# Performance work log

Hardware: AMD Instinct MI355X
Metric: run time of the kernel (lower is better)

## Reference

```python
import jax, jax.numpy as jnp
import numpy as np

LEAKY_SLOPE = 0.01  # torch nn.LeakyReLU default

def leaky_relu(x):
    return jnp.where(x >= 0, x, LEAKY_SLOPE * x)

def setup_inputs() -> dict:
    key = jax.random.key(0)
    ks = jax.random.split(key, 11)
    B, F, C_IN, H, K, D = 2048, 512, 3, 64, 8, 128  # batch, features, expand, layer_conf[0], bucket_num, bucket_dim
    ASR, MM, OUT = 128, 768, 256
    proj_in = ASR + MM + F * D
    inp = {
        "stat_features": jax.random.uniform(ks[0], (B, F), dtype=jnp.float32),
        "asr_embeddings": jax.random.normal(ks[1], (B, ASR), dtype=jnp.float32),
        "mm_embeddings": jax.random.normal(ks[2], (B, MM), dtype=jnp.float32),
        "linear1_w": jax.random.normal(ks[3], (F, C_IN, H), dtype=jnp.float32) * (1.0 / np.sqrt(C_IN)),
        "linear1_b": jax.random.normal(ks[4], (F, 1, H), dtype=jnp.float32),
        "linear2_w": jax.random.normal(ks[5], (F, H, K), dtype=jnp.float32) * (1.0 / np.sqrt(H)),
        "linear2_b": jax.random.normal(ks[6], (F, 1, K), dtype=jnp.float32),
        "tau": jnp.ones((F, 1, K), dtype=jnp.float32),
        "emb": jax.random.normal(ks[7], (F, K, D), dtype=jnp.float32),
        "proj_w": jax.random.normal(ks[8], (OUT, proj_in), dtype=jnp.float32) * (1.0 / np.sqrt(proj_in)),
        "proj_b": jax.random.normal(ks[9], (OUT,), dtype=jnp.float32) * 0.01,
    }
    return inp

def reference(stat_features, asr_embeddings, mm_embeddings,
              linear1_w, linear1_b, linear2_w, linear2_b, tau, emb,
              proj_w, proj_b):
    # sanitize: NaN -> 0, negatives -> 0
    x = stat_features
    x = jnp.where(jnp.isnan(x) | (x < 0.0), 0.0, x)  # [B, F]

    # auto_dis: per-feature tiny MLP. x is expanded to 3 identical copies -> [B,F,1,3]
    # matmul with [F,3,H] == einsum over the 3 copies.
    B, F = x.shape
    x3 = jnp.broadcast_to(x[:, :, None], (B, F, 3))           # [B,F,3]
    h = jnp.einsum('bfc,fch->bfh', x3, linear1_w) + linear1_b[:, 0, :]  # [B,F,H]
    h = jnp.where(h >= 0, h, LEAKY_SLOPE * h)
    s = jnp.einsum('bfh,fhk->bfk', h, linear2_w) + linear2_b[:, 0, :]   # [B,F,K]
    s = jnp.where(s >= 0, s, LEAKY_SLOPE * s)
    s = s * tau[:, 0, :]
    p = jax.nn.softmax(s, axis=-1)                            # [B,F,K]
    y = jnp.einsum('bfk,fkd->bfd', p, emb)                    # [B,F,D]
    y = y.reshape(B, -1)                                      # [B, F*D] (fc = Identity)

    z = jnp.concatenate([asr_embeddings, mm_embeddings, y], axis=1)
    out = jax.nn.relu(z @ proj_w.T + proj_b)                  # [B, 256]
    return out
```

## Files before the change

kernel.cpp:

```cpp
#include <hip/hip_runtime.h>
#include <hip/hip_bf16.h>
#include <math.h>

#define LEAKY 0.01f
#define B_    2048
#define F_    512
#define H_    64
#define K_    8
#define D_    128
#define ASR_  128
#define MM_   768
#define OUT_  256
#define PROJ_IN 66432
#define ZK    4992
#define NSPLIT 8


typedef unsigned short u16;
typedef u16   u16x8 __attribute__((ext_vector_type(8)));
typedef short s16x8 __attribute__((ext_vector_type(8)));
typedef float f32x4 __attribute__((ext_vector_type(4)));

__device__ __forceinline__ u16 f2bf(float x) {
  unsigned int u = __float_as_uint(x);
  u += 0x7fffu + ((u >> 16) & 1u);
  return (u16)(u >> 16);
}

#define PRODUCER_BLOCKS (512 + 1024 + 896 + 224)
#define PWS 132

__global__ __launch_bounds__(256) void producer_kernel(
    const float* __restrict__ stat, const float* __restrict__ w1,
    const float* __restrict__ b1v, const float* __restrict__ w2,
    const float* __restrict__ b2v, const float* __restrict__ tauv,
    const float* __restrict__ pw, const float* __restrict__ emb,
    const float* __restrict__ asr, const float* __restrict__ mm,
    u16* __restrict__ A0, u16* __restrict__ Pf, u16* __restrict__ Wn) {
  __shared__ __align__(16) char smem[15616];
  const int bid = blockIdx.x;
  const int t = threadIdx.x;

  if (bid < 512) {
    const int f0 = (bid >> 3) * 8;
    const int o0 = (bid & 7) * 32;
    float* s_pw = (float*)smem;
    const int fl = t >> 5, k = (t >> 2) & 7, dq = t & 3;
    float4 e[8];
    {
      const float* ep = emb + ((size_t)(f0 + fl) * 8 + k) * 128 + dq * 32;
      #pragma unroll
      for (int j = 0; j < 8; ++j) e[j] = *(const float4*)(ep + j * 4);
    }
    const int cf = t >> 5, cd = (t & 31) * 4;
    const float* pwbase = pw + 896 + (size_t)f0 * 128 + (size_t)(o0)*PROJ_IN + t * 4;
    float4 nxt = *(const float4*)(pwbase);
    for (int r = 0; r < 32; ++r) {
      float* buf = s_pw + (r & 1) * (8 * PWS);
      *(float4*)(buf + cf * PWS + cd) = nxt;
      __syncthreads();
      if (r + 1 < 32) nxt = *(const float4*)(pwbase + (size_t)(r + 1) * PROJ_IN);
      const float* pp = buf + fl * PWS + dq * 32;
      float g = 0.f;
      #pragma unroll
      for (int j = 0; j < 8; ++j) {
        float4 p4 = *(const float4*)(pp + j * 4);
        g = fmaf(e[j].x, p4.x, g);
        g = fmaf(e[j].y, p4.y, g);
        g = fmaf(e[j].z, p4.z, g);
        g = fmaf(e[j].w, p4.w, g);
      }
      g += __shfl_xor(g, 1);
      g += __shfl_xor(g, 2);
      if (dq == 0)
        Wn[(size_t)(o0 + r) * ZK + 896 + (f0 + fl) * 8 + k] = f2bf(g);
    }
  } else if (bid < 1536) {
    const int pb = bid - 512;
    const int f0 = (pb & 127) * 4;
    const int b0 = (pb >> 7) * 256;
    float* s_w1s = (float*)(smem);
    float* s_b1  = (float*)(smem + 1024);
    float* s_w2  = (float*)(smem + 2048);
    float* s_b2  = (float*)(smem + 10240);
    float* s_tau = (float*)(smem + 10368);
    float* s_x   = (float*)(smem + 10496);
    {
      int fl = t >> 6, h = t & 63;
      const float* wf = w1 + (size_t)(f0 + fl) * 192;
      s_w1s[fl * 64 + h] = wf[h] + wf[64 + h] + wf[128 + h];
      s_b1[fl * 64 + h] = b1v[(size_t)(f0 + fl) * 64 + h];
    }
    for (int i = t; i < 4 * 512; i += 256) {
      int fl = i >> 9, idx = i & 511;
      s_w2[fl * 512 + idx] = w2[(size_t)(f0 + fl) * 512 + idx];
    }
    if (t < 32) {
      s_b2[t]  = b2v[f0 * 8 + t];
      s_tau[t] = tauv[f0 * 8 + t];
    }
    for (int p = 0; p < 4; ++p) {
      int i = p * 256 + t;
      int r = i >> 2, fl = i & 3;
      float v = stat[(size_t)(b0 + r) * F_ + f0 + fl];
      s_x[r * 5 + fl] = (v >= 0.f) ? v : 0.f;
    }
    __syncthreads();

    const int w = t >> 6;
    const int lane = t & 63;
    const float* w1p = s_w1s + w * 64;
    const float* b1p = s_b1 + w * 64;
    const float* w2p = s_w2 + w * 512;
    float x[4];
    #pragma unroll
    for (int p = 0; p < 4; ++p) x[p] = s_x[(lane + 64 * p) * 5 + w];
    float acc[4][8] = {{0.f}};
    #pragma unroll 4
    for (int i = 0; i < 64; ++i) {
      float wv = w1p[i], bv = b1p[i];
      float4 wa = *(const float4*)(w2p + i * 8);
      float4 wb = *(const float4*)(w2p + i * 8 + 4);
      #pragma unroll
      for (int p = 0; p < 4; ++p) {
        float h0 = fmaf(x[p], wv, bv);
        float h = fmaf(LEAKY, fminf(h0, 0.f), fmaxf(h0, 0.f));
        acc[p][0] = fmaf(h, wa.x, acc[p][0]);
        acc[p][1] = fmaf(h, wa.y, acc[p][1]);
        acc[p][2] = fmaf(h, wa.z, acc[p][2]);
        acc[p][3] = fmaf(h, wa.w, acc[p][3]);
        acc[p][4] = fmaf(h, wb.x, acc[p][4]);
        acc[p][5] = fmaf(h, wb.y, acc[p][5]);
        acc[p][6] = fmaf(h, wb.z, acc[p][6]);
        acc[p][7] = fmaf(h, wb.w, acc[p][7]);
      }
    }
    #pragma unroll
    for (int p = 0; p < 4; ++p) {
      float s[K_];
      float m = -1e30f;
      #pragma unroll
      for (int kk = 0; kk < K_; ++kk) {
        float v = acc[p][kk] + s_b2[w * 8 + kk];
        v = (v >= 0.f) ? v : LEAKY * v;
        v *= s_tau[w * 8 + kk];
        s[kk] = v;
        m = fmaxf(m, v);
      }
      float sum = 0.f;
      #pragma unroll
      for (int kk = 0; kk < K_; ++kk) { s[kk] = __expf(s[kk] - m); sum += s[kk]; }
      float inv = 1.f / sum;
      u16x8 hv;
      #pragma unroll
      for (int kk = 0; kk < K_; ++kk) hv[kk] = f2bf(s[kk] * inv);
      *(u16x8*)(Pf + ((size_t)(f0 + w) * B_ + b0 + lane + 64 * p) * 8) = hv;
    }
  } else if (bid < 2432) {
    const int item = bid - 1536;
    const int cidx = item * 256 + t;
    const int r = cidx / 112, c = cidx % 112;
    float4 v0, v1;
    if (c < 16) {
      const float* s = asr + (size_t)r * ASR_ + c * 8;
      v0 = *(const float4*)(s); v1 = *(const float4*)(s + 4);
    } else {
      const float* s = mm + (size_t)r * MM_ + (c - 16) * 8;
      v0 = *(const float4*)(s); v1 = *(const float4*)(s + 4);
    }
    u16x8 hv = {f2bf(v0.x), f2bf(v0.y), f2bf(v0.z), f2bf(v0.w),
                f2bf(v1.x), f2bf(v1.y), f2bf(v1.z), f2bf(v1.w)};
    *(u16x8*)(A0 + (size_t)r * 896 + c * 8) = hv;
  } else {
    const int item = bid - 2432;
    #pragma unroll
    for (int rr = 0; rr < 4; ++rr) {
      int idx = item * 1024 + rr * 256 + t;
      int o = idx / 896, j = idx % 896;
      Wn[(size_t)o * ZK + j] = f2bf(pw[(size_t)o * PROJ_IN + j]);
    }
  }
}

#define SAS 72
__global__ __launch_bounds__(256) void gemm_kernel(
    const u16* __restrict__ A0, const u16* __restrict__ Pf,
    const u16* __restrict__ Wn, float* __restrict__ part) {
  const int bm0 = blockIdx.x * 64;
  const int bn0 = blockIdx.y * 64;
  const int kz  = blockIdx.z;
  const int it0 = kz * 10;
  const int itn = (kz == 7) ? 8 : 10;
  __shared__ u16 sA[64 * SAS];
  __shared__ u16 sB[64 * SAS];
  const int t = threadIdx.x;
  const int w = t >> 6, L = t & 63;
  const int l16 = L & 15, q8 = (L >> 4) * 8;
  const int wm = (w >> 1) * 32, wn = (w & 1) * 32;
  const int row = t >> 2, lk = t & 3;
  const int pp = t >> 5, pg = t & 31;
  f32x4 acc[2][2] = {{{0.f,0.f,0.f,0.f},{0.f,0.f,0.f,0.f}},
                     {{0.f,0.f,0.f,0.f},{0.f,0.f,0.f,0.f}}};
  u16x8 ra[2], rb[2];

#define LOAD_TILES(IT)                                                        \
  {                                                                           \
    const int k0_ = (IT) * 64;                                                \
    if (k0_ < 896) {                                                          \
      const u16* s_ = A0 + (size_t)(bm0 + row) * 896 + k0_ + lk * 8;          \
      ra[0] = *(const u16x8*)(s_);                                            \
      ra[1] = *(const u16x8*)(s_ + 32);                                       \
    } else {                                                                  \
      const int fb_ = (k0_ - 896) >> 3;                                       \
      const u16* s_ = Pf + ((size_t)(fb_ + pp) * B_ + bm0 + pg) * 8;          \
      ra[0] = *(const u16x8*)(s_);                                            \
      ra[1] = *(const u16x8*)(s_ + 256);                        \
    }                                                                         \
    const u16* sb_ = Wn + (size_t)(bn0 + row) * ZK + k0_ + lk * 8;            \
    rb[0] = *(const u16x8*)(sb_);                                             \
    rb[1] = *(const u16x8*)(sb_ + 32);                                        \
  }

#define STORE_TILES(IT)                                                       \
  {                                                                           \
    if ((IT) * 64 < 896) {                                                    \
      *(u16x8*)&sA[row * SAS + lk * 8]      = ra[0];                          \
      *(u16x8*)&sA[row * SAS + lk * 8 + 32] = ra[1];                          \
    } else {                                                                  \
      *(u16x8*)&sA[pg * SAS + pp * 8]        = ra[0];                         \
      *(u16x8*)&sA[(pg + 32) * SAS + pp * 8] = ra[1];                         \
    }                                                                         \
    *(u16x8*)&sB[row * SAS + lk * 8]      = rb[0];                            \
    *(u16x8*)&sB[row * SAS + lk * 8 + 32] = rb[1];                            \
  }

  LOAD_TILES(it0);
  for (int it = it0; it < it0 + itn; ++it) {
    __syncthreads();
    STORE_TILES(it);
    __syncthreads();
    if (it + 1 < it0 + itn) LOAD_TILES(it + 1);
    #pragma unroll
    for (int ks = 0; ks < 2; ++ks) {
      s16x8 a0 = *(const s16x8*)&sA[(wm + l16) * SAS + ks * 32 + q8];
      s16x8 a1 = *(const s16x8*)&sA[(wm + 16 + l16) * SAS + ks * 32 + q8];
      s16x8 b0 = *(const s16x8*)&sB[(wn + l16) * SAS + ks * 32 + q8];
      s16x8 b1 = *(const s16x8*)&sB[(wn + 16 + l16) * SAS + ks * 32 + q8];
      acc[0][0] = __builtin_amdgcn_mfma_f32_16x16x32_bf16(a0, b0, acc[0][0], 0, 0, 0);
      acc[0][1] = __builtin_amdgcn_mfma_f32_16x16x32_bf16(a0, b1, acc[0][1], 0, 0, 0);
      acc[1][0] = __builtin_amdgcn_mfma_f32_16x16x32_bf16(a1, b0, acc[1][0], 0, 0, 0);
      acc[1][1] = __builtin_amdgcn_mfma_f32_16x16x32_bf16(a1, b1, acc[1][1], 0, 0, 0);
    }
  }
#undef LOAD_TILES
#undef STORE_TILES

  float* dst = part + (size_t)kz * B_ * OUT_;
  #pragma unroll
  for (int mf = 0; mf < 2; ++mf) {
    const int r0 = bm0 + wm + mf * 16 + (L >> 4) * 4;
    #pragma unroll
    for (int nf = 0; nf < 2; ++nf) {
      const int col = bn0 + wn + nf * 16 + l16;
      #pragma unroll
      for (int i = 0; i < 4; ++i)
        dst[(size_t)(r0 + i) * OUT_ + col] = acc[mf][nf][i];
    }
  }
}

__global__ __launch_bounds__(256) void combine_kernel(
    const float* __restrict__ part, const float* __restrict__ pb,
    float* __restrict__ out) {
  const int idx4 = (blockIdx.x * 256 + threadIdx.x) * 4;
  const int o = idx4 & (OUT_ - 1);
  float4 bv = *(const float4*)(pb + o);
  float4 r = bv;
  #pragma unroll
  for (int kz = 0; kz < NSPLIT; ++kz) {
    float4 a = *(const float4*)(part + (size_t)kz * B_ * OUT_ + idx4);
    r.x += a.x; r.y += a.y; r.z += a.z; r.w += a.w;
  }
  r.x = r.x > 0.f ? r.x : 0.f;
  r.y = r.y > 0.f ? r.y : 0.f;
  r.z = r.z > 0.f ? r.z : 0.f;
  r.w = r.w > 0.f ? r.w : 0.f;
  *(float4*)(out + idx4) = r;
}

extern "C" void kernel_launch(void* const* d_in, const int* in_sizes, int n_in,
                              void* d_out, int out_size, void* d_ws, size_t ws_size,
                              hipStream_t stream) {
  (void)in_sizes; (void)n_in; (void)out_size; (void)ws_size;
  const float* stat = (const float*)d_in[0];
  const float* asr  = (const float*)d_in[1];
  const float* mm   = (const float*)d_in[2];
  const float* w1   = (const float*)d_in[3];
  const float* b1   = (const float*)d_in[4];
  const float* w2   = (const float*)d_in[5];
  const float* b2   = (const float*)d_in[6];
  const float* tau  = (const float*)d_in[7];
  const float* emb  = (const float*)d_in[8];
  const float* pw   = (const float*)d_in[9];
  const float* pb   = (const float*)d_in[10];
  float* out = (float*)d_out;
  char* ws = (char*)d_ws;
  u16*   A0   = (u16*)(ws);
  u16*   Pf   = (u16*)(ws + 3670016);
  u16*   Wn   = (u16*)(ws + 20447232);
  float* part = (float*)(ws + 23003136);

  producer_kernel<<<PRODUCER_BLOCKS, 256, 0, stream>>>(
      stat, w1, b1, w2, b2, tau, pw, emb, asr, mm, A0, Pf, Wn);
  gemm_kernel<<<dim3(B_ / 64, OUT_ / 64, NSPLIT), 256, 0, stream>>>(
      A0, Pf, Wn, part);
  combine_kernel<<<B_ * OUT_ / 1024, 256, 0, stream>>>(part, pb, out);
}
```

Before: 161.7 us.

## Fuse split-K combine into GEMM via atomic counters and split weight-fold blocks

Removes the separate combine kernel. Each GEMM tile increments a per-tile atomic counter, and the last split-K block for that tile sums the partials, adds bias, applies ReLU and writes the output. The weight-folding producer blocks are split into twice as many blocks with 16 outputs each. The shared-memory layout is padded per dq segment to reduce bank conflicts, and a trailing barrier is added. Counters are zeroed inside the producer kernel. This trades one launch and a full pass over the partials for atomics and fences.

Result: slower. 319.3 us (+97.5%).

```diff
diff --git a/kernel.cpp b/kernel.cpp
--- a/kernel.cpp
+++ b/kernel.cpp
@@ -27,8 +27,9 @@
   return (u16)(u >> 16);
 }
 
-#define PRODUCER_BLOCKS (512 + 1024 + 896 + 224)
-#define PWS 132
+#define PRODUCER_BLOCKS (1024 + 1024 + 896 + 224)
+#define DQS 36
+#define FLS 176
 
 __global__ __launch_bounds__(256) void producer_kernel(
     const float* __restrict__ stat, const float* __restrict__ w1,
@@ -36,14 +37,15 @@
     const float* __restrict__ b2v, const float* __restrict__ tauv,
     const float* __restrict__ pw, const float* __restrict__ emb,
     const float* __restrict__ asr, const float* __restrict__ mm,
-    u16* __restrict__ A0, u16* __restrict__ Pf, u16* __restrict__ Wn) {
+    u16* __restrict__ A0, u16* __restrict__ Pf, u16* __restrict__ Wn,
+    int* __restrict__ cnt) {
   __shared__ __align__(16) char smem[15616];
   const int bid = blockIdx.x;
   const int t = threadIdx.x;
 
-  if (bid < 512) {
-    const int f0 = (bid >> 3) * 8;
-    const int o0 = (bid & 7) * 32;
+  if (bid < 1024) {
+    const int f0 = (bid >> 4) * 8;
+    const int o0 = (bid & 15) * 16;
     float* s_pw = (float*)smem;
     const int fl = t >> 5, k = (t >> 2) & 7, dq = t & 3;
     float4 e[8];
@@ -52,15 +54,15 @@
       #pragma unroll
       for (int j = 0; j < 8; ++j) e[j] = *(const float4*)(ep + j * 4);
     }
-    const int cf = t >> 5, cd = (t & 31) * 4;
-    const float* pwbase = pw + 896 + (size_t)f0 * 128 + (size_t)(o0)*PROJ_IN + t * 4;
+    const int cf = t >> 5, dqs = (t & 31) >> 3, js = t & 7;
+    const float* pwbase = pw + 896 + (size_t)f0 * 128 + (size_t)o0 * PROJ_IN + t * 4;
     float4 nxt = *(const float4*)(pwbase);
-    for (int r = 0; r < 32; ++r) {
-      float* buf = s_pw + (r & 1) * (8 * PWS);
-      *(float4*)(buf + cf * PWS + cd) = nxt;
+    for (int r = 0; r < 16; ++r) {
+      float* buf = s_pw + (r & 1) * (8 * FLS);
+      *(float4*)(buf + cf * FLS + dqs * DQS + js * 4) = nxt;
       __syncthreads();
-      if (r + 1 < 32) nxt = *(const float4*)(pwbase + (size_t)(r + 1) * PROJ_IN);
-      const float* pp = buf + fl * PWS + dq * 32;
+      if (r + 1 < 16) nxt = *(const float4*)(pwbase + (size_t)(r + 1) * PROJ_IN);
+      const float* pp = buf + fl * FLS + dq * DQS;
       float g = 0.f;
       #pragma unroll
       for (int j = 0; j < 8; ++j) {
@@ -74,9 +76,10 @@
       g += __shfl_xor(g, 2);
       if (dq == 0)
         Wn[(size_t)(o0 + r) * ZK + 896 + (f0 + fl) * 8 + k] = f2bf(g);
-    }
-  } else if (bid < 1536) {
-    const int pb = bid - 512;
+      __syncthreads();
+    }
+  } else if (bid < 2048) {
+    const int pb = bid - 1024;
     const int f0 = (pb & 127) * 4;
     const int b0 = (pb >> 7) * 256;
     float* s_w1s = (float*)(smem);
@@ -156,8 +159,8 @@
       for (int kk = 0; kk < K_; ++kk) hv[kk] = f2bf(s[kk] * inv);
       *(u16x8*)(Pf + ((size_t)(f0 + w) * B_ + b0 + lane + 64 * p) * 8) = hv;
     }
-  } else if (bid < 2432) {
-    const int item = bid - 1536;
+  } else if (bid < 2944) {
+    const int item = bid - 2048;
     const int cidx = item * 256 + t;
     const int r = cidx / 112, c = cidx % 112;
     float4 v0, v1;
@@ -172,7 +175,8 @@
                 f2bf(v1.x), f2bf(v1.y), f2bf(v1.z), f2bf(v1.w)};
     *(u16x8*)(A0 + (size_t)r * 896 + c * 8) = hv;
   } else {
-    const int item = bid - 2432;
+    const int item = bid - 2944;
+    if (item == 0 && t < 128) cnt[t] = 0;
     #pragma unroll
     for (int rr = 0; rr < 4; ++rr) {
       int idx = item * 1024 + rr * 256 + t;
@@ -185,7 +189,9 @@
 #define SAS 72
 __global__ __launch_bounds__(256) void gemm_kernel(
     const u16* __restrict__ A0, const u16* __restrict__ Pf,
-    const u16* __restrict__ Wn, float* __restrict__ part) {
+    const u16* __restrict__ Wn, const float* __restrict__ pb,
+    float* __restrict__ part, float* __restrict__ out,
+    int* __restrict__ cnt) {
   const int bm0 = blockIdx.x * 64;
   const int bn0 = blockIdx.y * 64;
   const int kz  = blockIdx.z;
@@ -193,6 +199,7 @@
   const int itn = (kz == 7) ? 8 : 10;
   __shared__ u16 sA[64 * SAS];
   __shared__ u16 sB[64 * SAS];
+  __shared__ int s_last;
   const int t = threadIdx.x;
   const int w = t >> 6, L = t & 63;
   const int l16 = L & 15, q8 = (L >> 4) * 8;
@@ -267,25 +274,37 @@
         dst[(size_t)(r0 + i) * OUT_ + col] = acc[mf][nf][i];
     }
   }
-}
-
-__global__ __launch_bounds__(256) void combine_kernel(
-    const float* __restrict__ part, const float* __restrict__ pb,
-    float* __restrict__ out) {
-  const int idx4 = (blockIdx.x * 256 + threadIdx.x) * 4;
-  const int o = idx4 & (OUT_ - 1);
-  float4 bv = *(const float4*)(pb + o);
-  float4 r = bv;
+
+  __threadfence();
+  __syncthreads();
+  if (t == 0) {
+    int old = __hip_atomic_fetch_add(&cnt[blockIdx.y * 32 + blockIdx.x], 1,
+                                     __ATOMIC_ACQ_REL, __HIP_MEMORY_SCOPE_AGENT);
+    s_last = (old == NSPLIT - 1);
+  }
+  __syncthreads();
+  if (!s_last) return;
+  __threadfence();
+
+  const int c4 = (t & 15) * 4;
+  const int r4 = (t >> 4) * 4;
+  float4 bv = *(const float4*)(pb + bn0 + c4);
   #pragma unroll
-  for (int kz = 0; kz < NSPLIT; ++kz) {
-    float4 a = *(const float4*)(part + (size_t)kz * B_ * OUT_ + idx4);
-    r.x += a.x; r.y += a.y; r.z += a.z; r.w += a.w;
-  }
-  r.x = r.x > 0.f ? r.x : 0.f;
-  r.y = r.y > 0.f ? r.y : 0.f;
-  r.z = r.z > 0.f ? r.z : 0.f;
-  r.w = r.w > 0.f ? r.w : 0.f;
-  *(float4*)(out + idx4) = r;
+  for (int i = 0; i < 4; ++i) {
+    const int rrow = bm0 + r4 + i;
+    float4 s = bv;
+    #pragma unroll
+    for (int z = 0; z < NSPLIT; ++z) {
+      float4 a = *(const float4*)(part + (size_t)z * B_ * OUT_ +
+                                  (size_t)rrow * OUT_ + bn0 + c4);
+      s.x += a.x; s.y += a.y; s.z += a.z; s.w += a.w;
+    }
+    s.x = s.x > 0.f ? s.x : 0.f;
+    s.y = s.y > 0.f ? s.y : 0.f;
+    s.z = s.z > 0.f ? s.z : 0.f;
+    s.w = s.w > 0.f ? s.w : 0.f;
+    *(float4*)(out + (size_t)rrow * OUT_ + bn0 + c4) = s;
+  }
 }
 
 extern "C" void kernel_launch(void* const* d_in, const int* in_sizes, int n_in,
@@ -309,10 +328,10 @@
   u16*   Pf   = (u16*)(ws + 3670016);
   u16*   Wn   = (u16*)(ws + 20447232);
   float* part = (float*)(ws + 23003136);
+  int*   cnt  = (int*)(ws + 39780352);
 
   producer_kernel<<<PRODUCER_BLOCKS, 256, 0, stream>>>(
-      stat, w1, b1, w2, b2, tau, pw, emb, asr, mm, A0, Pf, Wn);
+      stat, w1, b1, w2, b2, tau, pw, emb, asr, mm, A0, Pf, Wn, cnt);
   gemm_kernel<<<dim3(B_ / 64, OUT_ / 64, NSPLIT), 256, 0, stream>>>(
-      A0, Pf, Wn, part);
-  combine_kernel<<<B_ * OUT_ / 1024, 256, 0, stream>>>(part, pb, out);
+      A0, Pf, Wn, pb, part, out, cnt);
 }
```

## Fold emb into proj weights with register prefetch and ds_swizzle reductions, no LDS

Applied to the files above, without the earlier changes.

Reworks the producer branch that folds the bucket embedding into the projection weights. Each wave now covers two features, with half a wave per feature. Every lane loads a float4 of proj_w straight from global memory with a two-deep register prefetch, which removes the shared-memory staging and the per-row __syncthreads. The 32-lane dot product is reduced with ds_swizzle butterfly adds and written as one 8-wide bf16 store. The grid for this stage doubles to 1024 blocks with 16 output rows each, at the cost of more reduction instructions per output.

Result: no change. 162.5 us (+0.5%).

```diff
diff --git a/kernel.cpp b/kernel.cpp
--- a/kernel.cpp
+++ b/kernel.cpp
@@ -27,8 +27,13 @@
   return (u16)(u >> 16);
 }
 
-#define PRODUCER_BLOCKS (512 + 1024 + 896 + 224)
-#define PWS 132
+template <int PAT>
+__device__ __forceinline__ float swz_add(float x) {
+  int y = __builtin_amdgcn_ds_swizzle(__float_as_int(x), PAT);
+  return x + __int_as_float(y);
+}
+
+#define PRODUCER_BLOCKS (1024 + 1024 + 896 + 224)
 
 __global__ __launch_bounds__(256) void producer_kernel(
     const float* __restrict__ stat, const float* __restrict__ w1,
@@ -41,42 +46,50 @@
   const int bid = blockIdx.x;
   const int t = threadIdx.x;
 
-  if (bid < 512) {
-    const int f0 = (bid >> 3) * 8;
-    const int o0 = (bid & 7) * 32;
-    float* s_pw = (float*)smem;
-    const int fl = t >> 5, k = (t >> 2) & 7, dq = t & 3;
+  if (bid < 1024) {
+    const int wv = t >> 6, lane = t & 63;
+    const int fp = (bid >> 4) * 4 + wv;
+    const int o0 = (bid & 15) * 16;
+    const int f = fp * 2 + (lane >> 5);
     float4 e[8];
     {
-      const float* ep = emb + ((size_t)(f0 + fl) * 8 + k) * 128 + dq * 32;
-      #pragma unroll
-      for (int j = 0; j < 8; ++j) e[j] = *(const float4*)(ep + j * 4);
-    }
-    const int cf = t >> 5, cd = (t & 31) * 4;
-    const float* pwbase = pw + 896 + (size_t)f0 * 128 + (size_t)(o0)*PROJ_IN + t * 4;
-    float4 nxt = *(const float4*)(pwbase);
-    for (int r = 0; r < 32; ++r) {
-      float* buf = s_pw + (r & 1) * (8 * PWS);
-      *(float4*)(buf + cf * PWS + cd) = nxt;
-      __syncthreads();
-      if (r + 1 < 32) nxt = *(const float4*)(pwbase + (size_t)(r + 1) * PROJ_IN);
-      const float* pp = buf + fl * PWS + dq * 32;
-      float g = 0.f;
-      #pragma unroll
-      for (int j = 0; j < 8; ++j) {
-        float4 p4 = *(const float4*)(pp + j * 4);
-        g = fmaf(e[j].x, p4.x, g);
-        g = fmaf(e[j].y, p4.y, g);
-        g = fmaf(e[j].z, p4.z, g);
-        g = fmaf(e[j].w, p4.w, g);
-      }
-      g += __shfl_xor(g, 1);
-      g += __shfl_xor(g, 2);
-      if (dq == 0)
-        Wn[(size_t)(o0 + r) * ZK + 896 + (f0 + fl) * 8 + k] = f2bf(g);
-    }
-  } else if (bid < 1536) {
-    const int pb = bid - 512;
+      const float* ep = emb + (size_t)f * (K_ * D_) + (lane & 31) * 4;
+      #pragma unroll
+      for (int k = 0; k < 8; ++k) e[k] = *(const float4*)(ep + k * D_);
+    }
+    const float* base = pw + (size_t)o0 * PROJ_IN + 896 + fp * 256 + lane * 4;
+    float4 pv0 = *(const float4*)(base);
+    float4 pv1 = *(const float4*)(base + PROJ_IN);
+    #pragma unroll
+    for (int r = 0; r < 16; ++r) {
+      float4 cur = (r & 1) ? pv1 : pv0;
+      if (r + 2 < 16) {
+        float4 nv = *(const float4*)(base + (size_t)(r + 2) * PROJ_IN);
+        if (r & 1) pv1 = nv; else pv0 = nv;
+      }
+      float g[8];
+      #pragma unroll
+      for (int k = 0; k < 8; ++k) {
+        float s = e[k].x * cur.x;
+        s = fmaf(e[k].y, cur.y, s);
+        s = fmaf(e[k].z, cur.z, s);
+        s = fmaf(e[k].w, cur.w, s);
+        s = swz_add<0x041F>(s);
+        s = swz_add<0x081F>(s);
+        s = swz_add<0x101F>(s);
+        s = swz_add<0x201F>(s);
+        s = swz_add<0x401F>(s);
+        g[k] = s;
+      }
+      if ((lane & 31) == 0) {
+        u16x8 hv;
+        #pragma unroll
+        for (int k = 0; k < 8; ++k) hv[k] = f2bf(g[k]);
+        *(u16x8*)(Wn + (size_t)(o0 + r) * ZK + 896 + f * 8) = hv;
+      }
+    }
+  } else if (bid < 2048) {
+    const int pb = bid - 1024;
     const int f0 = (pb & 127) * 4;
     const int b0 = (pb >> 7) * 256;
     float* s_w1s = (float*)(smem);
@@ -156,8 +169,8 @@
       for (int kk = 0; kk < K_; ++kk) hv[kk] = f2bf(s[kk] * inv);
       *(u16x8*)(Pf + ((size_t)(f0 + w) * B_ + b0 + lane + 64 * p) * 8) = hv;
     }
-  } else if (bid < 2432) {
-    const int item = bid - 1536;
+  } else if (bid < 2944) {
+    const int item = bid - 2048;
     const int cidx = item * 256 + t;
     const int r = cidx / 112, c = cidx % 112;
     float4 v0, v1;
@@ -172,7 +185,7 @@
                 f2bf(v1.x), f2bf(v1.y), f2bf(v1.z), f2bf(v1.w)};
     *(u16x8*)(A0 + (size_t)r * 896 + c * 8) = hv;
   } else {
-    const int item = bid - 2432;
+    const int item = bid - 2944;
     #pragma unroll
     for (int rr = 0; rr < 4; ++rr) {
       int idx = item * 1024 + rr * 256 + t;
```
